# Optimization experiments

Hardware: AMD Instinct MI355X
Metric: run time of the kernel (lower is better)

The kernel has to match this reference:

```python
import jax, jax.numpy as jnp
import numpy as np

T, B, CIN, HW = 64, 32, 4, 116
GH = 128


def _conv(x, w, b, stride, pad):
    y = jax.lax.conv_general_dilated(
        x, w, (stride, stride), [(pad, pad), (pad, pad)],
        dimension_numbers=("NCHW", "OIHW", "NCHW"))
    return y if b is None else y + b[None, :, None, None]


def setup_inputs() -> dict:
    key = jax.random.key(0)
    ks = jax.random.split(key, 24)
    r = lambda i, shape, s: jax.random.normal(ks[i], shape, jnp.float32) * s
    return {
        "x": jax.random.normal(ks[0], (T * B, CIN, HW, HW), jnp.float32),
        "done": jax.random.uniform(ks[1], (T * B,), jnp.float32),
        "gru_state": jnp.zeros((1, B, GH), jnp.float32),
        # Nature-CNN backbone
        "c1w": r(2, (32, CIN, 8, 8), 0.05), "c1b": jnp.zeros((32,), jnp.float32),
        "c2w": r(3, (64, 32, 4, 4), 0.05), "c2b": jnp.zeros((64,), jnp.float32),
        "c3w": r(4, (64, 64, 3, 3), 0.05), "c3b": jnp.zeros((64,), jnp.float32),
        # CBAM
        "fc1w": r(5, (16, 64), 0.1), "fc2w": r(6, (64, 16), 0.1),
        "spw": r(7, (1, 2, 7, 7), 0.1),
        # spatial self-attention (dim=64, heads=4)
        "qkvw": r(8, (192, 64), 0.05), "projw": r(9, (64, 64), 0.05),
        "projb": jnp.zeros((64,), jnp.float32),
        # FC 2304 -> 256
        "fcw": r(10, (256, 2304), 0.02), "fcb": jnp.zeros((256,), jnp.float32),
        # GRU(256 -> 128), PyTorch layout (3H, in)/(3H, H), gate order r,z,n
        "wih": r(11, (3 * GH, 256), 0.05), "whh": r(12, (3 * GH, GH), 0.05),
        "bih": jnp.zeros((3 * GH,), jnp.float32), "bhh": jnp.zeros((3 * GH,), jnp.float32),
        # critic head
        "crw": r(13, (1, GH), 0.05), "crb": jnp.zeros((1,), jnp.float32),
    }


def reference(x, done, gru_state, c1w, c1b, c2w, c2b, c3w, c3b,
              fc1w, fc2w, spw, qkvw, projw, projb, fcw, fcb,
              wih, whh, bih, bhh, crw, crb):
    # conv backbone: (N,4,116,116) -> (N,64,6,6)
    h = jax.nn.relu(_conv(x, c1w, c1b, 4, 0))
    h = jax.nn.relu(_conv(h, c2w, c2b, 2, 0))
    h = jax.nn.relu(_conv(h, c3w, c3b, 2, 0))
    # CBAM channel attention
    mlp = lambda v: jax.nn.relu(v @ fc1w.T) @ fc2w.T
    ch_att = jax.nn.sigmoid(mlp(h.mean((2, 3))) + mlp(h.max((2, 3))))[:, :, None, None]
    h = h * ch_att
    # CBAM spatial attention
    sp_in = jnp.concatenate([h.mean(1, keepdims=True), h.max(1, keepdims=True)], axis=1)
    h = h * jax.nn.sigmoid(_conv(sp_in, spw, None, 1, 3))
    # spatial self-attention over 36 tokens of dim 64
    N, C, Hh, Ww = h.shape
    nh, hd = 4, C // 4
    tok = h.reshape(N, C, Hh * Ww).transpose(0, 2, 1)  # (N,36,64)
    qkv = (tok @ qkvw.T).reshape(N, Hh * Ww, 3, nh, hd).transpose(2, 0, 3, 1, 4)
    q, k, v = qkv[0], qkv[1], qkv[2]  # (N,heads,36,hd)
    att = jax.nn.softmax((q @ k.transpose(0, 1, 3, 2)) * hd ** -0.5, axis=-1)
    out = (att @ v).transpose(0, 2, 1, 3).reshape(N, Hh * Ww, C) @ projw.T + projb
    tok = tok + out
    h = tok.transpose(0, 2, 1).reshape(N, C, Hh, Ww)
    # FC(2304 -> 256)
    feat = jax.nn.relu(h.reshape(N, -1) @ fcw.T + fcb)
    # masked GRU scan: reshape into (T, B, 256)
    bsz = gru_state.shape[1]
    seq = feat.reshape(-1, bsz, 256)
    dn = done.reshape(-1, bsz)
    h0 = gru_state[0]

    def step(hc, xd):
        xt, dt = xd
        hc = (1.0 - dt)[:, None] * hc
        gx = xt @ wih.T + bih
        gh = hc @ whh.T + bhh
        xr, xz, xn = jnp.split(gx, 3, axis=-1)
        hr, hz, hn = jnp.split(gh, 3, axis=-1)
        rg = jax.nn.sigmoid(xr + hr)
        zg = jax.nn.sigmoid(xz + hz)
        ng = jnp.tanh(xn + rg * hn)
        hc = (1.0 - zg) * ng + zg * hc
        return hc, hc

    _, hs = jax.lax.scan(step, h0, (seq, dn))
    hidden = hs.reshape(-1, GH)  # (T*B, 128)
    return hidden @ crw.T + crb  # critic value (T*B, 1)
```

## Files before the change

### kernel.cpp

```cpp
#include <hip/hip_runtime.h>
#include <math.h>

typedef _Float16 f16;
typedef f16 f16x8 __attribute__((ext_vector_type(8)));
typedef f16 f16x2 __attribute__((ext_vector_type(2)));
typedef float f32x4 __attribute__((ext_vector_type(4)));

__global__ __launch_bounds__(256) void k_prep(const float* __restrict__ c1w,
                                              const float* __restrict__ c2w,
                                              const float* __restrict__ c3w,
                                              const float* __restrict__ fcw,
                                              const float* __restrict__ wih,
                                              const float* __restrict__ qkvw,
                                              const float* __restrict__ projw,
                                              f16* __restrict__ W1, f16* __restrict__ W2,
                                              f16* __restrict__ W3, f16* __restrict__ FCW,
                                              f16* __restrict__ WIH, f16* __restrict__ QKVW,
                                              f16* __restrict__ PROJW) {
    int i0 = blockIdx.x * 256 + threadIdx.x;
    if (i0 < 8192) {
        int n = i0 >> 8, k = i0 & 255;
        int kh = k >> 5, r = k & 31, c = r >> 3, kw = r & 7;
        W1[i0] = (f16)c1w[((n * 4 + c) * 8 + kh) * 8 + kw];
    } else if (i0 < 8192 + 32768) {
        int i = i0 - 8192;
        int n = i >> 9, k = i & 511;
        int kh = k >> 7, r = k & 127, kw = r >> 5, c = r & 31;
        W2[i] = (f16)c2w[((n * 32 + c) * 4 + kh) * 4 + kw];
    } else if (i0 < 8192 + 32768 + 36864) {
        int i = i0 - (8192 + 32768);
        int n = i / 576, k = i % 576;
        int kh = k / 192, r = k % 192, kw = r / 64, c = r & 63;
        W3[i] = (f16)c3w[((n * 64 + c) * 3 + kh) * 3 + kw];
    } else if (i0 < 8192 + 32768 + 36864 + 589824) {
        int i = i0 - (8192 + 32768 + 36864);
        int o = i / 2304, k = i % 2304, p = k >> 6, c = k & 63;
        FCW[i] = (f16)fcw[o * 2304 + c * 36 + p];
    } else if (i0 < 765952) {
        int i = i0 - (8192 + 32768 + 36864 + 589824);
        WIH[i] = (f16)wih[i];
    } else if (i0 < 765952 + 12288) {
        int i = i0 - 765952;
        QKVW[i] = (f16)(qkvw[i] * ((i < 4096) ? 0.25f : 1.f));
    } else if (i0 < 765952 + 12288 + 4096) {
        int i = i0 - (765952 + 12288);
        PROJW[i] = (f16)projw[i];
    }
}

template <int CINP, int KH, int KW, int STRIDE, int IW, int OW, int PPI, int NCH, bool SRCF32>
__global__ __launch_bounds__(256) void k_conv(const void* __restrict__ srcv,
                                              const f16* __restrict__ W,
                                              const float* __restrict__ bias,
                                              f16* __restrict__ dst) {
    constexpr int CK = KW * CINP;
    constexpr int KS = CK / 32;
    constexpr int NT = NCH / 16;
    constexpr int LA = CK + 8;
    constexpr int AUN = SRCF32 ? 64 * CINP : (64 * CK) / 8;
    constexpr int WUN = (NCH * CK) / 8;
    constexpr int ANU = (AUN + 255) / 256;
    constexpr int WNU = (WUN + 255) / 256;
    __shared__ f16 As[64 * LA];
    __shared__ f16 Bs[NCH * LA];
    const int tid = threadIdx.x;
    const int wave = tid >> 6, lane = tid & 63;
    int bid = blockIdx.x;
    int nwg = gridDim.x;
    int swz = ((nwg & 7) == 0) ? ((bid & 7) * (nwg >> 3) + (bid >> 3)) : bid;
    const int m0 = swz * 64;

    int aGB[ANU], aLO[ANU];
#pragma unroll
    for (int j = 0; j < ANU; j++) {
        int u = tid + j * 256;
        if (u < AUN) {
            if (SRCF32) {
                int px = u / CINP, c = u % CINP;
                int m = m0 + px, n = m / PPI, pp = m % PPI, oy = pp / OW, ox = pp % OW;
                aGB[j] = ((n * CINP + c) * IW + oy * STRIDE) * IW + ox * STRIDE;
                aLO[j] = px * LA + c * 8;
            } else {
                constexpr int SPP = CK / 8;
                int px = u / SPP, seg = u % SPP;
                int m = m0 + px, n = m / PPI, pp = m % PPI, oy = pp / OW, ox = pp % OW;
                aGB[j] = ((n * IW + oy * STRIDE) * IW + ox * STRIDE) * CINP + seg * 8;
                aLO[j] = px * LA + seg * 8;
            }
        }
    }
    int wGB[WNU], wLO[WNU];
#pragma unroll
    for (int j = 0; j < WNU; j++) {
        int u = tid + j * 256;
        if (u < WUN) {
            constexpr int SPP = CK / 8;
            int n = u / SPP, seg = u % SPP;
            wGB[j] = n * (KH * CK) + seg * 8;
            wLO[j] = n * LA + seg * 8;
        }
    }

    f32x4 acc[NT] = {};
    const f16* ap = As + (wave * 16 + (lane & 15)) * LA + (lane >> 4) * 8;
    const f16* bp = Bs + (lane & 15) * LA + (lane >> 4) * 8;

    for (int kh = 0; kh < KH; kh++) {
        __syncthreads();
#pragma unroll
        for (int j = 0; j < ANU; j++) {
            int u = tid + j * 256;
            if (u < AUN) {
                if (SRCF32) {
                    const float* s = (const float*)srcv + aGB[j] + kh * IW;
                    float4 v0 = *(const float4*)s;
                    float4 v1 = *(const float4*)(s + 4);
                    f16x8 h;
                    h[0] = (f16)v0.x; h[1] = (f16)v0.y; h[2] = (f16)v0.z; h[3] = (f16)v0.w;
                    h[4] = (f16)v1.x; h[5] = (f16)v1.y; h[6] = (f16)v1.z; h[7] = (f16)v1.w;
                    *(f16x8*)(As + aLO[j]) = h;
                } else {
                    const f16* s = (const f16*)srcv + aGB[j] + kh * (IW * CINP);
                    *(f16x8*)(As + aLO[j]) = *(const f16x8*)s;
                }
            }
        }
#pragma unroll
        for (int j = 0; j < WNU; j++) {
            int u = tid + j * 256;
            if (u < WUN)
                *(f16x8*)(Bs + wLO[j]) = *(const f16x8*)(W + wGB[j] + kh * CK);
        }
        __syncthreads();
#pragma unroll
        for (int ks = 0; ks < KS; ks++) {
            f16x8 af = *(const f16x8*)(ap + ks * 32);
#pragma unroll
            for (int nt = 0; nt < NT; nt++) {
                f16x8 bf = *(const f16x8*)(bp + nt * 16 * LA + ks * 32);
                acc[nt] = __builtin_amdgcn_mfma_f32_16x16x32_f16(af, bf, acc[nt], 0, 0, 0);
            }
        }
    }
    __syncthreads();
    {
        int rrow = wave * 16 + ((lane >> 4) << 2);
        int col = lane & 15;
#pragma unroll
        for (int nt = 0; nt < NT; nt++) {
            float bb = bias[nt * 16 + col];
#pragma unroll
            for (int r = 0; r < 4; r++) {
                float v = acc[nt][r] + bb;
                As[(rrow + r) * NCH + nt * 16 + col] = (f16)fmaxf(v, 0.f);
            }
        }
    }
    __syncthreads();
    constexpr int OUN = 64 * NCH / 8;
    for (int u = tid; u < OUN; u += 256) {
        int px = u / (NCH / 8), seg = u % (NCH / 8);
        *(f16x8*)(dst + (size_t)(m0 + px) * NCH + seg * 8) = *(const f16x8*)(As + px * NCH + seg * 8);
    }
}

template <bool RELU, bool OUTF32, bool RESID>
__global__ __launch_bounds__(256) void k_gemm16(const f16* __restrict__ A,
                                                const f16* __restrict__ W,
                                                const float* __restrict__ bias,
                                                const f16* __restrict__ R,
                                                void* __restrict__ Cv, int N, int K) {
    __shared__ f16 As[64 * 72];
    __shared__ f16 Bs[64 * 72];
    int tid = threadIdx.x, wave = tid >> 6, lane = tid & 63;
    int n0 = blockIdx.x * 64, m0 = blockIdx.y * 64;
    f32x4 acc[4] = {};
    const f16* ap = As + (wave * 16 + (lane & 15)) * 72 + (lane >> 4) * 8;
    const f16* bp = Bs + (lane & 15) * 72 + (lane >> 4) * 8;
    int arow = tid >> 3, aseg = tid & 7;
    for (int k0 = 0; k0 < K; k0 += 64) {
        __syncthreads();
        *(f16x8*)(As + arow * 72 + aseg * 8) = *(const f16x8*)(A + (size_t)(m0 + arow) * K + k0 + aseg * 8);
        *(f16x8*)(As + (arow + 32) * 72 + aseg * 8) = *(const f16x8*)(A + (size_t)(m0 + arow + 32) * K + k0 + aseg * 8);
        *(f16x8*)(Bs + arow * 72 + aseg * 8) = *(const f16x8*)(W + (size_t)(n0 + arow) * K + k0 + aseg * 8);
        *(f16x8*)(Bs + (arow + 32) * 72 + aseg * 8) = *(const f16x8*)(W + (size_t)(n0 + arow + 32) * K + k0 + aseg * 8);
        __syncthreads();
#pragma unroll
        for (int ks = 0; ks < 2; ks++) {
            f16x8 af = *(const f16x8*)(ap + ks * 32);
#pragma unroll
            for (int nt = 0; nt < 4; nt++) {
                f16x8 bf = *(const f16x8*)(bp + nt * 16 * 72 + ks * 32);
                acc[nt] = __builtin_amdgcn_mfma_f32_16x16x32_f16(af, bf, acc[nt], 0, 0, 0);
            }
        }
    }
    int mrow = m0 + wave * 16 + ((lane >> 4) << 2);
    int col = n0 + (lane & 15);
#pragma unroll
    for (int nt = 0; nt < 4; nt++) {
        float bb = bias[col + nt * 16];
#pragma unroll
        for (int r = 0; r < 4; r++) {
            float v = acc[nt][r] + bb;
            if (RESID) v += (float)R[(size_t)(mrow + r) * N + col + nt * 16];
            if (RELU) v = fmaxf(v, 0.f);
            if (OUTF32) ((float*)Cv)[(size_t)(mrow + r) * N + col + nt * 16] = v;
            else ((f16*)Cv)[(size_t)(mrow + r) * N + col + nt * 16] = (f16)v;
        }
    }
}

__global__ __launch_bounds__(256) void k_gate(f16* __restrict__ h3,
                                              const float* __restrict__ fc1w,
                                              const float* __restrict__ fc2w,
                                              const float* __restrict__ spw) {
    __shared__ float tok[4][36][67];
    __shared__ float pm[4][64], px[4][64], hml[4][32], chv[4][64];
    __shared__ float spm[4][36], spx[4][36], gsp[4][36];
    int s = threadIdx.x >> 6, lane = threadIdx.x & 63;
    f16* hb = h3 + (size_t)(blockIdx.x * 4 + s) * 2304;
    for (int i = lane; i < 2304; i += 64) tok[s][i >> 6][i & 63] = (float)hb[i];
    __syncthreads();
    {
        float m = 0.f, mx = -1e30f;
        for (int p = 0; p < 36; p++) { float v = tok[s][p][lane]; m += v; mx = fmaxf(mx, v); }
        pm[s][lane] = m * (1.f / 36.f); px[s][lane] = mx;
    }
    __syncthreads();
    if (lane < 32) {
        int j = lane & 15;
        const float* srcv = (lane < 16) ? pm[s] : px[s];
        float acc = 0.f;
        for (int c = 0; c < 64; c++) acc += fc1w[j * 64 + c] * srcv[c];
        hml[s][lane] = fmaxf(acc, 0.f);
    }
    __syncthreads();
    {
        float acc = 0.f;
        for (int j = 0; j < 16; j++) acc += fc2w[lane * 16 + j] * (hml[s][j] + hml[s][16 + j]);
        chv[s][lane] = 1.f / (1.f + expf(-acc));
    }
    __syncthreads();
    if (lane < 36) {
        float m = 0.f, mx = -1e30f;
        for (int c = 0; c < 64; c++) {
            float v = tok[s][lane][c] * chv[s][c];
            tok[s][lane][c] = v; m += v; mx = fmaxf(mx, v);
        }
        spm[s][lane] = m * (1.f / 64.f); spx[s][lane] = mx;
    }
    __syncthreads();
    if (lane < 36) {
        int y = lane / 6, x = lane % 6;
        float acc = 0.f;
        for (int dy = 0; dy < 7; dy++) {
            int yy = y + dy - 3; if (yy < 0 || yy > 5) continue;
            for (int dx = 0; dx < 7; dx++) {
                int xx = x + dx - 3; if (xx < 0 || xx > 5) continue;
                int pp = yy * 6 + xx;
                acc += spw[dy * 7 + dx] * spm[s][pp] + spw[49 + dy * 7 + dx] * spx[s][pp];
            }
        }
        gsp[s][lane] = 1.f / (1.f + expf(-acc));
    }
    __syncthreads();
    for (int i = lane; i < 2304; i += 64) {
        int p = i >> 6;
        hb[i] = (f16)(tok[s][p][i & 63] * gsp[s][p]);
    }
}

__global__ __launch_bounds__(256) void k_attn(const f16* __restrict__ qkv,
                                              f16* __restrict__ attout) {
    __shared__ f16 t[36][200];
    __shared__ f16 att[144][40];
    int tid = threadIdx.x;
    const f16* src = qkv + (size_t)blockIdx.x * 36 * 192;
    for (int i = tid; i < 864; i += 256) {
        int p = i / 24, seg = i % 24;
        *(f16x8*)(&t[p][seg * 8]) = *(const f16x8*)(src + p * 192 + seg * 8);
    }
    __syncthreads();
    for (int i = tid; i < 5184; i += 256) {
        int h = i / 1296, r = i % 1296, p = r / 36, p2 = r % 36;
        f16x8 qa = *(const f16x8*)(&t[p][h * 16]);
        f16x8 qb = *(const f16x8*)(&t[p][h * 16 + 8]);
        f16x8 ka = *(const f16x8*)(&t[p2][64 + h * 16]);
        f16x8 kb = *(const f16x8*)(&t[p2][64 + h * 16 + 8]);
        float s = 0.f;
#pragma unroll
        for (int j = 0; j < 8; j++)
            s += (float)qa[j] * (float)ka[j] + (float)qb[j] * (float)kb[j];
        att[h * 36 + p][p2] = (f16)s;
    }
    __syncthreads();
    if (tid < 144) {
        float mx = -1e30f;
        for (int j = 0; j < 36; j++) mx = fmaxf(mx, (float)att[tid][j]);
        float sum = 0.f; float e[36];
        for (int j = 0; j < 36; j++) { float v = __expf((float)att[tid][j] - mx); e[j] = v; sum += v; }
        float inv = 1.f / sum;
        for (int j = 0; j < 36; j++) att[tid][j] = (f16)(e[j] * inv);
    }
    __syncthreads();
    for (int i = tid; i < 1152; i += 256) {
        int p = i >> 5, cp = i & 31, c0 = cp * 2, h = c0 >> 4;
        const f16* ar = &att[h * 36 + p][0];
        float s0 = 0.f, s1 = 0.f;
        for (int p2 = 0; p2 < 36; p2++) {
            float a = (float)ar[p2];
            f16x2 vv = *(const f16x2*)(&t[p2][128 + c0]);
            s0 += a * (float)vv[0]; s1 += a * (float)vv[1];
        }
        f16x2 o; o[0] = (f16)s0; o[1] = (f16)s1;
        *(f16x2*)(attout + (size_t)blockIdx.x * 2304 + p * 64 + c0) = o;
    }
}

__global__ __launch_bounds__(256, 1) void k_gru(const float* __restrict__ GX,
                                                const float* __restrict__ done,
                                                const float* __restrict__ h0,
                                                const float* __restrict__ whh,
                                                const float* __restrict__ bhh,
                                                float* __restrict__ hs) {
    __shared__ float hlds[2][16][132];
    __shared__ float dlds[2048];
    const int tid = threadIdx.x;
    const int wave = tid >> 6, lane = tid & 63;
    const int lr = lane & 15, lq = lane >> 4;
    const int b0 = blockIdx.x * 16;

    for (int i = tid; i < 2048; i += 256) dlds[i] = done[i];
    for (int i = tid; i < 2048; i += 256) hlds[0][i >> 7][i & 127] = h0[(size_t)b0 * 128 + i];

    f16x8 wf[6][4];
#pragma unroll
    for (int j = 0; j < 6; j++) {
        int n = (wave + 4 * j) * 16 + lr;
#pragma unroll
        for (int ks = 0; ks < 4; ks++) {
            const float* s = whh + (size_t)n * 128 + ks * 32 + lq * 8;
            float4 v0 = *(const float4*)s, v1 = *(const float4*)(s + 4);
            f16x8 h;
            h[0] = (f16)v0.x; h[1] = (f16)v0.y; h[2] = (f16)v0.z; h[3] = (f16)v0.w;
            h[4] = (f16)v1.x; h[5] = (f16)v1.y; h[6] = (f16)v1.z; h[7] = (f16)v1.w;
            wf[j][ks] = h;
        }
    }
    float bh[3][2];
#pragma unroll
    for (int g = 0; g < 3; g++)
#pragma unroll
        for (int hh = 0; hh < 2; hh++)
            bh[g][hh] = bhh[g * 128 + (wave + 4 * hh) * 16 + lr];

    int cur = 0;
    float pxA[2][4][3], pxB[2][4][3];

    auto loadpx = [&](int t, float (&px)[2][4][3]) {
#pragma unroll
        for (int hh = 0; hh < 2; hh++) {
            int d = (wave + 4 * hh) * 16 + lr;
#pragma unroll
            for (int r = 0; r < 4; r++) {
                const float* g = GX + (size_t)(t * 32 + b0 + lq * 4 + r) * 384 + d;
                px[hh][r][0] = g[0]; px[hh][r][1] = g[128]; px[hh][r][2] = g[256];
            }
        }
    };

    auto step = [&](int t, float (&pxU)[2][4][3], float (&pxN)[2][4][3]) {
        __syncthreads();
        float dtA = 1.f - dlds[t * 32 + b0 + lr];
        f16x8 af[4];
#pragma unroll
        for (int ks = 0; ks < 4; ks++) {
            const float* hr = &hlds[cur][lr][ks * 32 + lq * 8];
            float4 v0 = *(const float4*)hr, v1 = *(const float4*)(hr + 4);
            f16x8 h;
            h[0] = (f16)(v0.x * dtA); h[1] = (f16)(v0.y * dtA);
            h[2] = (f16)(v0.z * dtA); h[3] = (f16)(v0.w * dtA);
            h[4] = (f16)(v1.x * dtA); h[5] = (f16)(v1.y * dtA);
            h[6] = (f16)(v1.z * dtA); h[7] = (f16)(v1.w * dtA);
            af[ks] = h;
        }
        float dtb[4];
#pragma unroll
        for (int r = 0; r < 4; r++) dtb[r] = 1.f - dlds[t * 32 + b0 + lq * 4 + r];
        float hcm[2][4];
#pragma unroll
        for (int hh = 0; hh < 2; hh++) {
            int d = (wave + 4 * hh) * 16 + lr;
#pragma unroll
            for (int r = 0; r < 4; r++)
                hcm[hh][r] = hlds[cur][lq * 4 + r][d] * dtb[r];
        }
        int tn = t + 1 < 64 ? t + 1 : 63;
        loadpx(tn, pxN);
        f32x4 acc[6] = {};
#pragma unroll
        for (int ks = 0; ks < 4; ks++) {
#pragma unroll
            for (int j = 0; j < 6; j++)
                acc[j] = __builtin_amdgcn_mfma_f32_16x16x32_f16(af[ks], wf[j][ks], acc[j], 0, 0, 0);
        }
        int nxt = cur ^ 1;
#pragma unroll
        for (int hh = 0; hh < 2; hh++) {
            int d = (wave + 4 * hh) * 16 + lr;
#pragma unroll
            for (int r = 0; r < 4; r++) {
                float sr = acc[0 + hh][r] + bh[0][hh];
                float sz = acc[2 + hh][r] + bh[1][hh];
                float sn = acc[4 + hh][r] + bh[2][hh];
                float rg = 1.f / (1.f + __expf(-(pxU[hh][r][0] + sr)));
                float zg = 1.f / (1.f + __expf(-(pxU[hh][r][1] + sz)));
                float a = pxU[hh][r][2] + rg * sn;
                float ng = 2.f / (1.f + __expf(-2.f * a)) - 1.f;
                float hnew = (1.f - zg) * ng + zg * hcm[hh][r];
                hlds[nxt][lq * 4 + r][d] = hnew;
                hs[(size_t)(t * 32 + b0 + lq * 4 + r) * 128 + d] = hnew;
            }
        }
        cur = nxt;
    };

    loadpx(0, pxA);
    for (int t = 0; t < 64; t += 2) {
        step(t, pxA, pxB);
        step(t + 1, pxB, pxA);
    }
}

__global__ __launch_bounds__(256) void k_critic(const float* __restrict__ hs,
                                                const float* __restrict__ crw,
                                                const float* __restrict__ crb,
                                                float* __restrict__ out) {
    int wave = threadIdx.x >> 6, lane = threadIdx.x & 63;
    int row = blockIdx.x * 4 + wave;
    const float* hr = hs + (size_t)row * 128;
    float s = hr[lane] * crw[lane] + hr[64 + lane] * crw[64 + lane];
#pragma unroll
    for (int off = 32; off; off >>= 1) s += __shfl_down(s, off);
    if (lane == 0) out[row] = s + crb[0];
}

extern "C" void kernel_launch(void* const* d_in, const int* in_sizes, int n_in,
                              void* d_out, int out_size, void* d_ws, size_t ws_size,
                              hipStream_t stream) {
    const float* x     = (const float*)d_in[0];
    const float* done  = (const float*)d_in[1];
    const float* gru0  = (const float*)d_in[2];
    const float* c1w   = (const float*)d_in[3];
    const float* c1b   = (const float*)d_in[4];
    const float* c2w   = (const float*)d_in[5];
    const float* c2b   = (const float*)d_in[6];
    const float* c3w   = (const float*)d_in[7];
    const float* c3b   = (const float*)d_in[8];
    const float* fc1w  = (const float*)d_in[9];
    const float* fc2w  = (const float*)d_in[10];
    const float* spw   = (const float*)d_in[11];
    const float* qkvw  = (const float*)d_in[12];
    const float* projw = (const float*)d_in[13];
    const float* projb = (const float*)d_in[14];
    const float* fcw   = (const float*)d_in[15];
    const float* fcb   = (const float*)d_in[16];
    const float* wih   = (const float*)d_in[17];
    const float* whh   = (const float*)d_in[18];
    const float* bih   = (const float*)d_in[19];
    const float* bhh   = (const float*)d_in[20];
    const float* crw   = (const float*)d_in[21];
    const float* crb   = (const float*)d_in[22];
    float* out = (float*)d_out;

    f16* h1   = (f16*)d_ws;
    f16* h2   = h1 + 51380224ull;
    f16* h3   = h2 + 22151168ull;
    f16* f256 = h3 + 4718592ull;
    f16* W1   = f256 + 524288ull;
    f16* W2   = W1 + 8192;
    f16* W3   = W2 + 32768;
    f16* FCW  = W3 + 36864;
    f16* WIH  = FCW + 589824;
    f16* QKVW = WIH + 98304;
    f16* PROJW = QKVW + 12288;
    float* zb  = (float*)(PROJW + 4096);
    float* gxb = zb + 192;
    float* hsb = gxb + 786432;
    f16* qkv    = h1;
    f16* attout = h1 + 14155776ull;

    k_prep<<<3056, 256, 0, stream>>>(c1w, c2w, c3w, fcw, wih, qkvw, projw,
                                     W1, W2, W3, FCW, WIH, QKVW, PROJW);
    hipMemsetAsync(zb, 0, 768, stream);

    k_conv<4, 8, 8, 4, 116, 28, 784, 32, true><<<25088, 256, 0, stream>>>(x, W1, c1b, h1);
    k_conv<32, 4, 4, 2, 28, 13, 169, 64, false><<<5408, 256, 0, stream>>>(h1, W2, c2b, h2);
    k_conv<64, 3, 3, 2, 13, 6, 36, 64, false><<<1152, 256, 0, stream>>>(h2, W3, c3b, h3);
    k_gate<<<512, 256, 0, stream>>>(h3, fc1w, fc2w, spw);
    k_gemm16<false, false, false><<<dim3(3, 1152), 256, 0, stream>>>(h3, QKVW, zb, nullptr, qkv, 192, 64);
    k_attn<<<2048, 256, 0, stream>>>(qkv, attout);
    k_gemm16<false, false, true><<<dim3(1, 1152), 256, 0, stream>>>(attout, PROJW, projb, h3, h3, 64, 64);
    k_gemm16<true, false, false><<<dim3(4, 32), 256, 0, stream>>>(h3, FCW, fcb, nullptr, f256, 256, 2304);
    k_gemm16<false, true, false><<<dim3(6, 32), 256, 0, stream>>>(f256, WIH, bih, nullptr, gxb, 384, 256);
    k_gru<<<2, 256, 0, stream>>>(gxb, done, gru0, whh, bhh, hsb);
    k_critic<<<512, 256, 0, stream>>>(hsb, crw, crb, out);
}
```

Baseline: 1.078 ms.

## Add per-image conv1 kernel with LDS row window and widen GRU to 512 threads

Conv1 now runs as its own kernel with one block per image. Each block keeps a rolling 12-row fp16 window of the input in LDS, so every input row is read and converted once per image instead of being reloaded for each output pixel and kernel row. The output is staged through LDS to get coalesced stores. Separately, the GRU kernel uses 8 waves, each owning one 16-column hidden slice across the three gates, which halves per-wave MFMA and epilogue work on the serial recurrence. The costs are more syncthreads per output row in conv1 and a grid of only 2048 blocks that loop serially over 28 rows.

```diff
diff --git a/kernel.cpp b/kernel.cpp
--- a/kernel.cpp
+++ b/kernel.cpp
@@ -3,6 +3,7 @@
 
 typedef _Float16 f16;
 typedef f16 f16x8 __attribute__((ext_vector_type(8)));
+typedef f16 f16x4 __attribute__((ext_vector_type(4)));
 typedef f16 f16x2 __attribute__((ext_vector_type(2)));
 typedef float f32x4 __attribute__((ext_vector_type(4)));
 
@@ -48,8 +49,80 @@
     }
 }
 
-template <int CINP, int KH, int KW, int STRIDE, int IW, int OW, int PPI, int NCH, bool SRCF32>
-__global__ __launch_bounds__(256) void k_conv(const void* __restrict__ srcv,
+__global__ __launch_bounds__(256) void k_conv1(const float* __restrict__ x,
+                                               const f16* __restrict__ W,
+                                               const float* __restrict__ bias,
+                                               f16* __restrict__ dst) {
+    __shared__ __attribute__((aligned(16))) f16 As[32 * 264];
+    __shared__ __attribute__((aligned(16))) f16 Bs[32 * 264];
+    __shared__ __attribute__((aligned(16))) f16 win[4][12][120];
+    const int tid = threadIdx.x;
+    const int wave = tid >> 6, lane = tid & 63;
+    const int lr = lane & 15, lq = lane >> 4;
+    const int n = blockIdx.x;
+    const int mt = wave >> 1, nt = wave & 1;
+
+    for (int u = tid; u < 1024; u += 256)
+        *(f16x8*)(Bs + (u >> 5) * 264 + (u & 31) * 8) = *(const f16x8*)(W + u * 8);
+    for (int u = tid; u < 132; u += 256) {
+        f16x8 z = {};
+        *(f16x8*)(As + 28 * 264 + u * 8) = z;
+    }
+    const float bb = bias[nt * 16 + lr];
+    const f16* ap = As + (mt * 16 + lr) * 264 + lq * 8;
+    const f16* bp = Bs + (nt * 16 + lr) * 264 + lq * 8;
+    const float* xb = x + (size_t)n * 4 * 116 * 116;
+
+    for (int oy = 0; oy < 28; oy++) {
+        int r0 = (oy == 0) ? 0 : oy * 4 + 4;
+        int nu = (oy == 0) ? 928 : 464;
+        for (int u = tid; u < nu; u += 256) {
+            int ch4 = u % 29, rc = u / 29;
+            int c = rc & 3, r = rc >> 2;
+            int iy = r0 + r;
+            float4 v = *(const float4*)(xb + ((size_t)c * 116 + iy) * 116 + ch4 * 4);
+            f16x4 h;
+            h[0] = (f16)v.x; h[1] = (f16)v.y; h[2] = (f16)v.z; h[3] = (f16)v.w;
+            *(f16x4*)(&win[c][iy % 12][ch4 * 4]) = h;
+        }
+        __syncthreads();
+        for (int u = tid; u < 896; u += 256) {
+            int px = u >> 5, rr = u & 31;
+            int kh = rr >> 2, c = rr & 3;
+            const f16* s = &win[c][(oy * 4 + kh) % 12][px * 4];
+            f16x4 a0 = *(const f16x4*)s;
+            f16x4 a1 = *(const f16x4*)(s + 4);
+            f16x8 h8;
+            h8[0] = a0[0]; h8[1] = a0[1]; h8[2] = a0[2]; h8[3] = a0[3];
+            h8[4] = a1[0]; h8[5] = a1[1]; h8[6] = a1[2]; h8[7] = a1[3];
+            *(f16x8*)(As + px * 264 + kh * 32 + c * 8) = h8;
+        }
+        __syncthreads();
+        f32x4 acc = {};
+#pragma unroll
+        for (int ks = 0; ks < 8; ks++) {
+            f16x8 af = *(const f16x8*)(ap + ks * 32);
+            f16x8 bf = *(const f16x8*)(bp + ks * 32);
+            acc = __builtin_amdgcn_mfma_f32_16x16x32_f16(af, bf, acc, 0, 0, 0);
+        }
+        __syncthreads();
+#pragma unroll
+        for (int r = 0; r < 4; r++) {
+            int px = mt * 16 + lq * 4 + r;
+            if (px < 28)
+                As[px * 32 + nt * 16 + lr] = (f16)fmaxf(acc[r] + bb, 0.f);
+        }
+        __syncthreads();
+        if (tid < 112) {
+            int px = tid >> 2, seg = tid & 3;
+            *(f16x8*)(dst + ((size_t)n * 784 + oy * 28 + px) * 32 + seg * 8) =
+                *(const f16x8*)(As + px * 32 + seg * 8);
+        }
+    }
+}
+
+template <int CINP, int KH, int KW, int STRIDE, int IW, int OW, int PPI, int NCH>
+__global__ __launch_bounds__(256) void k_conv(const f16* __restrict__ src,
                                               const f16* __restrict__ W,
                                               const float* __restrict__ bias,
                                               f16* __restrict__ dst) {
@@ -57,7 +130,7 @@
     constexpr int KS = CK / 32;
     constexpr int NT = NCH / 16;
     constexpr int LA = CK + 8;
-    constexpr int AUN = SRCF32 ? 64 * CINP : (64 * CK) / 8;
+    constexpr int AUN = (64 * CK) / 8;
     constexpr int WUN = (NCH * CK) / 8;
     constexpr int ANU = (AUN + 255) / 256;
     constexpr int WNU = (WUN + 255) / 256;
@@ -75,18 +148,11 @@
     for (int j = 0; j < ANU; j++) {
         int u = tid + j * 256;
         if (u < AUN) {
-            if (SRCF32) {
-                int px = u / CINP, c = u % CINP;
-                int m = m0 + px, n = m / PPI, pp = m % PPI, oy = pp / OW, ox = pp % OW;
-                aGB[j] = ((n * CINP + c) * IW + oy * STRIDE) * IW + ox * STRIDE;
-                aLO[j] = px * LA + c * 8;
-            } else {
-                constexpr int SPP = CK / 8;
-                int px = u / SPP, seg = u % SPP;
-                int m = m0 + px, n = m / PPI, pp = m % PPI, oy = pp / OW, ox = pp % OW;
-                aGB[j] = ((n * IW + oy * STRIDE) * IW + ox * STRIDE) * CINP + seg * 8;
-                aLO[j] = px * LA + seg * 8;
-            }
+            constexpr int SPP = CK / 8;
+            int px = u / SPP, seg = u % SPP;
+            int m = m0 + px, n = m / PPI, pp = m % PPI, oy = pp / OW, ox = pp % OW;
+            aGB[j] = ((n * IW + oy * STRIDE) * IW + ox * STRIDE) * CINP + seg * 8;
+            aLO[j] = px * LA + seg * 8;
         }
     }
     int wGB[WNU], wLO[WNU];
@@ -110,20 +176,8 @@
 #pragma unroll
         for (int j = 0; j < ANU; j++) {
             int u = tid + j * 256;
-            if (u < AUN) {
-                if (SRCF32) {
-                    const float* s = (const float*)srcv + aGB[j] + kh * IW;
-                    float4 v0 = *(const float4*)s;
-                    float4 v1 = *(const float4*)(s + 4);
-                    f16x8 h;
-                    h[0] = (f16)v0.x; h[1] = (f16)v0.y; h[2] = (f16)v0.z; h[3] = (f16)v0.w;
-                    h[4] = (f16)v1.x; h[5] = (f16)v1.y; h[6] = (f16)v1.z; h[7] = (f16)v1.w;
-                    *(f16x8*)(As + aLO[j]) = h;
-                } else {
-                    const f16* s = (const f16*)srcv + aGB[j] + kh * (IW * CINP);
-                    *(f16x8*)(As + aLO[j]) = *(const f16x8*)s;
-                }
-            }
+            if (u < AUN)
+                *(f16x8*)(As + aLO[j]) = *(const f16x8*)(src + aGB[j] + kh * (IW * CINP));
         }
 #pragma unroll
         for (int j = 0; j < WNU; j++) {
@@ -318,7 +372,7 @@
     }
 }
 
-__global__ __launch_bounds__(256, 1) void k_gru(const float* __restrict__ GX,
+__global__ __launch_bounds__(512, 1) void k_gru(const float* __restrict__ GX,
                                                 const float* __restrict__ done,
                                                 const float* __restrict__ h0,
                                                 const float* __restrict__ whh,
@@ -330,47 +384,40 @@
     const int wave = tid >> 6, lane = tid & 63;
     const int lr = lane & 15, lq = lane >> 4;
     const int b0 = blockIdx.x * 16;
-
-    for (int i = tid; i < 2048; i += 256) dlds[i] = done[i];
-    for (int i = tid; i < 2048; i += 256) hlds[0][i >> 7][i & 127] = h0[(size_t)b0 * 128 + i];
-
-    f16x8 wf[6][4];
-#pragma unroll
-    for (int j = 0; j < 6; j++) {
-        int n = (wave + 4 * j) * 16 + lr;
+    const int d = wave * 16 + lr;
+
+    for (int i = tid; i < 2048; i += 512) dlds[i] = done[i];
+    for (int i = tid; i < 2048; i += 512) hlds[0][i >> 7][i & 127] = h0[(size_t)b0 * 128 + i];
+
+    f16x8 wf[3][4];
+#pragma unroll
+    for (int g = 0; g < 3; g++) {
 #pragma unroll
         for (int ks = 0; ks < 4; ks++) {
-            const float* s = whh + (size_t)n * 128 + ks * 32 + lq * 8;
+            const float* s = whh + (size_t)(g * 128 + d) * 128 + ks * 32 + lq * 8;
             float4 v0 = *(const float4*)s, v1 = *(const float4*)(s + 4);
             f16x8 h;
             h[0] = (f16)v0.x; h[1] = (f16)v0.y; h[2] = (f16)v0.z; h[3] = (f16)v0.w;
             h[4] = (f16)v1.x; h[5] = (f16)v1.y; h[6] = (f16)v1.z; h[7] = (f16)v1.w;
-            wf[j][ks] = h;
-        }
-    }
-    float bh[3][2];
-#pragma unroll
-    for (int g = 0; g < 3; g++)
-#pragma unroll
-        for (int hh = 0; hh < 2; hh++)
-            bh[g][hh] = bhh[g * 128 + (wave + 4 * hh) * 16 + lr];
+            wf[g][ks] = h;
+        }
+    }
+    float bh[3];
+#pragma unroll
+    for (int g = 0; g < 3; g++) bh[g] = bhh[g * 128 + d];
 
     int cur = 0;
-    float pxA[2][4][3], pxB[2][4][3];
-
-    auto loadpx = [&](int t, float (&px)[2][4][3]) {
-#pragma unroll
-        for (int hh = 0; hh < 2; hh++) {
-            int d = (wave + 4 * hh) * 16 + lr;
-#pragma unroll
-            for (int r = 0; r < 4; r++) {
-                const float* g = GX + (size_t)(t * 32 + b0 + lq * 4 + r) * 384 + d;
-                px[hh][r][0] = g[0]; px[hh][r][1] = g[128]; px[hh][r][2] = g[256];
-            }
+    float pxA[4][3], pxB[4][3];
+
+    auto loadpx = [&](int t, float (&px)[4][3]) {
+#pragma unroll
+        for (int r = 0; r < 4; r++) {
+            const float* g = GX + (size_t)(t * 32 + b0 + lq * 4 + r) * 384 + d;
+            px[r][0] = g[0]; px[r][1] = g[128]; px[r][2] = g[256];
         }
     };
 
-    auto step = [&](int t, float (&pxU)[2][4][3], float (&pxN)[2][4][3]) {
+    auto step = [&](int t, float (&pxU)[4][3], float (&pxN)[4][3]) {
         __syncthreads();
         float dtA = 1.f - dlds[t * 32 + b0 + lr];
         f16x8 af[4];
@@ -385,43 +432,34 @@
             h[6] = (f16)(v1.z * dtA); h[7] = (f16)(v1.w * dtA);
             af[ks] = h;
         }
-        float dtb[4];
-#pragma unroll
-        for (int r = 0; r < 4; r++) dtb[r] = 1.f - dlds[t * 32 + b0 + lq * 4 + r];
-        float hcm[2][4];
-#pragma unroll
-        for (int hh = 0; hh < 2; hh++) {
-            int d = (wave + 4 * hh) * 16 + lr;
-#pragma unroll
-            for (int r = 0; r < 4; r++)
-                hcm[hh][r] = hlds[cur][lq * 4 + r][d] * dtb[r];
+        float hcm[4];
+#pragma unroll
+        for (int r = 0; r < 4; r++) {
+            float dtb = 1.f - dlds[t * 32 + b0 + lq * 4 + r];
+            hcm[r] = hlds[cur][lq * 4 + r][d] * dtb;
         }
         int tn = t + 1 < 64 ? t + 1 : 63;
         loadpx(tn, pxN);
-        f32x4 acc[6] = {};
+        f32x4 acc[3] = {};
 #pragma unroll
         for (int ks = 0; ks < 4; ks++) {
 #pragma unroll
-            for (int j = 0; j < 6; j++)
-                acc[j] = __builtin_amdgcn_mfma_f32_16x16x32_f16(af[ks], wf[j][ks], acc[j], 0, 0, 0);
+            for (int g = 0; g < 3; g++)
+                acc[g] = __builtin_amdgcn_mfma_f32_16x16x32_f16(af[ks], wf[g][ks], acc[g], 0, 0, 0);
         }
         int nxt = cur ^ 1;
 #pragma unroll
-        for (int hh = 0; hh < 2; hh++) {
-            int d = (wave + 4 * hh) * 16 + lr;
-#pragma unroll
-            for (int r = 0; r < 4; r++) {
-                float sr = acc[0 + hh][r] + bh[0][hh];
-                float sz = acc[2 + hh][r] + bh[1][hh];
-                float sn = acc[4 + hh][r] + bh[2][hh];
-                float rg = 1.f / (1.f + __expf(-(pxU[hh][r][0] + sr)));
-                float zg = 1.f / (1.f + __expf(-(pxU[hh][r][1] + sz)));
-                float a = pxU[hh][r][2] + rg * sn;
-                float ng = 2.f / (1.f + __expf(-2.f * a)) - 1.f;
-                float hnew = (1.f - zg) * ng + zg * hcm[hh][r];
-                hlds[nxt][lq * 4 + r][d] = hnew;
-                hs[(size_t)(t * 32 + b0 + lq * 4 + r) * 128 + d] = hnew;
-            }
+        for (int r = 0; r < 4; r++) {
+            float sr = acc[0][r] + bh[0];
+            float sz = acc[1][r] + bh[1];
+            float sn = acc[2][r] + bh[2];
+            float rg = 1.f / (1.f + __expf(-(pxU[r][0] + sr)));
+            float zg = 1.f / (1.f + __expf(-(pxU[r][1] + sz)));
+            float a = pxU[r][2] + rg * sn;
+            float ng = 2.f / (1.f + __expf(-2.f * a)) - 1.f;
+            float hnew = (1.f - zg) * ng + zg * hcm[r];
+            hlds[nxt][lq * 4 + r][d] = hnew;
+            hs[(size_t)(t * 32 + b0 + lq * 4 + r) * 128 + d] = hnew;
         }
         cur = nxt;
     };
@@ -495,15 +533,15 @@
                                      W1, W2, W3, FCW, WIH, QKVW, PROJW);
     hipMemsetAsync(zb, 0, 768, stream);
 
-    k_conv<4, 8, 8, 4, 116, 28, 784, 32, true><<<25088, 256, 0, stream>>>(x, W1, c1b, h1);
-    k_conv<32, 4, 4, 2, 28, 13, 169, 64, false><<<5408, 256, 0, stream>>>(h1, W2, c2b, h2);
-    k_conv<64, 3, 3, 2, 13, 6, 36, 64, false><<<1152, 256, 0, stream>>>(h2, W3, c3b, h3);
+    k_conv1<<<2048, 256, 0, stream>>>(x, W1, c1b, h1);
+    k_conv<32, 4, 4, 2, 28, 13, 169, 64><<<5408, 256, 0, stream>>>(h1, W2, c2b, h2);
+    k_conv<64, 3, 3, 2, 13, 6, 36, 64><<<1152, 256, 0, stream>>>(h2, W3, c3b, h3);
     k_gate<<<512, 256, 0, stream>>>(h3, fc1w, fc2w, spw);
     k_gemm16<false, false, false><<<dim3(3, 1152), 256, 0, stream>>>(h3, QKVW, zb, nullptr, qkv, 192, 64);
     k_attn<<<2048, 256, 0, stream>>>(qkv, attout);
     k_gemm16<false, false, true><<<dim3(1, 1152), 256, 0, stream>>>(attout, PROJW, projb, h3, h3, 64, 64);
     k_gemm16<true, false, false><<<dim3(4, 32), 256, 0, stream>>>(h3, FCW, fcb, nullptr, f256, 256, 2304);
     k_gemm16<false, true, false><<<dim3(6, 32), 256, 0, stream>>>(f256, WIH, bih, nullptr, gxb, 384, 256);
-    k_gru<<<2, 256, 0, stream>>>(gxb, done, gru0, whh, bhh, hsb);
+    k_gru<<<2, 512, 0, stream>>>(gxb, done, gru0, whh, bhh, hsb);
     k_critic<<<512, 256, 0, stream>>>(hsb, crw, crb, out);
 }
```

Measured after the change: 1.075 ms. About the same (-0.2%).
